# Optimization experiments

Measured on AMD Instinct MI355X. Metric: run time of the kernel, lower is better.

Reference implementation:

```python
import jax, jax.numpy as jnp
import numpy as np
from jax import lax

N, T, V, E, H, D, B = 16384, 16, 10000, 256, 256, 512, 128


def setup_inputs() -> dict:
    key = jax.random.key(0)
    ks = jax.random.split(key, 12)
    tok = jax.random.randint(ks[0], (N, T), 1, V)
    lens = jax.random.randint(ks[1], (N,), 4, T + 1)
    tok = jnp.where(jnp.arange(T)[None, :] < lens[:, None], tok, 0)  # pad_id = 0
    ast_path_len = jnp.full((B,), N // B, dtype=jnp.int32)  # 128 paths per sample
    u = lambda k, s: jax.random.uniform(k, s, jnp.float32, -0.1, 0.1)
    emb = u(ks[2], (V, E)).at[0].set(0.0)  # padding_idx=0 row zeroed
    return {
        "ast_path": tok,
        "ast_path_len": ast_path_len,
        "emb": emb,
        "W_ih_f": u(ks[3], (4 * H, E)), "W_hh_f": u(ks[4], (4 * H, H)), "b_f": u(ks[5], (4 * H,)),
        "W_ih_b": u(ks[6], (4 * H, E)), "W_hh_b": u(ks[7], (4 * H, H)), "b_b": u(ks[8], (4 * H,)),
        "W_lin": u(ks[9], (D, 2 * H)), "b_lin": jnp.zeros((D,), jnp.float32),
    }


def _lstm_final_h(x_tm, lens, W_ih, W_hh, b, reverse):
    # x_tm: [T, N, E]; returns final hidden state [N, H] honoring per-seq length
    n = x_tm.shape[1]
    h0 = jnp.zeros((n, H), x_tm.dtype)

    def step(carry, xt):
        h, c = carry
        x, t = xt
        gates = x @ W_ih.T + h @ W_hh.T + b  # [N, 4H]
        i, f, g, o = jnp.split(gates, 4, axis=-1)
        c_new = jax.nn.sigmoid(f) * c + jax.nn.sigmoid(i) * jnp.tanh(g)
        h_new = jax.nn.sigmoid(o) * jnp.tanh(c_new)
        m = (t < lens)[:, None]  # packed-sequence semantics: frozen past length
        return (jnp.where(m, h_new, h), jnp.where(m, c_new, c)), None

    (h, _), _ = lax.scan(step, (h0, h0), (x_tm, jnp.arange(x_tm.shape[0])), reverse=reverse)
    return h


def reference(ast_path, ast_path_len, emb, W_ih_f, W_hh_f, b_f, W_ih_b, W_hh_b, b_b, W_lin, b_lin):
    lens = (ast_path != 0).sum(axis=-1)  # pad_id = 0
    x = emb[ast_path]                     # [N, T, E]; dropout is identity at eval
    x_tm = jnp.swapaxes(x, 0, 1)          # [T, N, E]
    h_fwd = _lstm_final_h(x_tm, lens, W_ih_f, W_hh_f, b_f, reverse=False)
    h_bwd = _lstm_final_h(x_tm, lens, W_ih_b, W_hh_b, b_b, reverse=True)
    h_n = jnp.concatenate([h_fwd, h_bwd], axis=1)        # [N, 2H]
    repr_ = h_n @ W_lin.T + b_lin                         # [N, D]
    # segment-mean pooling over path groups (replaces the Python loop)
    n_paths = repr_.shape[0]
    seg_ids = jnp.repeat(jnp.arange(ast_path_len.shape[0]), ast_path_len,
                         total_repeat_length=n_paths)
    sums = jax.ops.segment_sum(repr_, seg_ids, num_segments=ast_path_len.shape[0])
    pooled = sums / ast_path_len[:, None].astype(repr_.dtype)  # [B, D]
    norm = jnp.sqrt(jnp.sum(pooled * pooled, axis=-1, keepdims=True))
    return pooled / jnp.maximum(norm, 1e-5)
```

## Files before the change

### kernel.cpp

```cpp
#include <hip/hip_runtime.h>
#include <stdint.h>

#define N_SEQ 16384
#define T_LEN 16
#define E_DIM 256
#define H_DIM 256
#define B_SAMP 128
#define V_SIZE 10000

typedef __bf16 bf16x8 __attribute__((ext_vector_type(8)));
typedef float  f32x4  __attribute__((ext_vector_type(4)));
typedef unsigned short u16x8 __attribute__((ext_vector_type(8)));
typedef unsigned short ush;

__device__ __forceinline__ ush f2bf(float x) {
  unsigned int u = __float_as_uint(x);
  u = (u + 0x7fffu + ((u >> 16) & 1u)) >> 16;
  return (ush)u;
}
__device__ __forceinline__ float bf2f(ush v) {
  return __uint_as_float(((unsigned int)v) << 16);
}
__device__ __forceinline__ float sigmoidf_(float x) {
  return 1.0f / (1.0f + __expf(-x));
}
__device__ __forceinline__ float tanhf_(float x) {
  float e = __expf(2.0f * x);
  return 1.0f - 2.0f / (e + 1.0f);
}
__device__ __forceinline__ void glds16(const void* g, const void* l) {
  __builtin_amdgcn_global_load_lds(
      (const __attribute__((address_space(1))) unsigned int*)g,
      (__attribute__((address_space(3))) unsigned int*)l, 16, 0, 0);
}


__global__ __launch_bounds__(256) void k_lens(const int* __restrict__ tok, int* __restrict__ lens) {
  int n = blockIdx.x * 256 + threadIdx.x;
  const int* r = tok + n * T_LEN;
  int c = 0;
#pragma unroll
  for (int t = 0; t < T_LEN; ++t) c += (r[t] != 0);
  lens[n] = c;
}

__global__ __launch_bounds__(256) void k_hist(const int* __restrict__ lens, int* __restrict__ hist) {
  __shared__ int lh[17];
  if (threadIdx.x < 17) lh[threadIdx.x] = 0;
  __syncthreads();
  atomicAdd(&lh[lens[blockIdx.x * 256 + threadIdx.x]], 1);
  __syncthreads();
  if (threadIdx.x < 17) atomicAdd(&hist[threadIdx.x], lh[threadIdx.x]);
}

__global__ void k_offsets(const int* __restrict__ hist, int* __restrict__ cursor,
                          int* __restrict__ cnts_f, int* __restrict__ cnts_b) {
  if (threadIdx.x == 0) {
    int off = 0;
    for (int l = 16; l >= 0; --l) { cursor[l] = off; off += hist[l]; }
    for (int t = 0; t < 16; ++t) {
      int cf = 0, cb = 0;
      for (int l = t; l <= 16; ++l) cf += hist[l];
      for (int l = t + 1; l <= 16; ++l) cb += hist[l];
      cnts_f[t] = cf;
      cnts_b[t] = cb;
    }
  }
}

__global__ __launch_bounds__(256) void k_scatter(const int* __restrict__ tok, const int* __restrict__ lens,
                                                 int* __restrict__ cursor,
                                                 int* __restrict__ pinv, int* __restrict__ plens,
                                                 int* __restrict__ tokperm) {
  int n = blockIdx.x * 256 + threadIdx.x;
  int l = lens[n];
  int pos = atomicAdd(&cursor[l], 1);
  pinv[n] = pos;
  plens[pos] = l;
#pragma unroll
  for (int t = 0; t < T_LEN; ++t) tokperm[t * N_SEQ + pos] = tok[n * T_LEN + t];
}

__global__ __launch_bounds__(256) void k_embcvt(const float* __restrict__ emb, ush* __restrict__ out) {
  int i = blockIdx.x * 256 + threadIdx.x;
  out[i] = f2bf(emb[i]);
}

__global__ __launch_bounds__(256) void k_wprep(const float* __restrict__ Wih_f, const float* __restrict__ Whh_f,
                                               const float* __restrict__ Wih_b, const float* __restrict__ Whh_b,
                                               ush* __restrict__ wihp_f, ush* __restrict__ wihp_b,
                                               ush* __restrict__ whhp_f, ush* __restrict__ whhp_b) {
  int id = blockIdx.x * 256 + threadIdx.x;
  int mat = id >> 19;
  int dir = (id >> 18) & 1;
  int rem = id & ((1 << 18) - 1);
  int p = rem >> 8;
  int k = rem & 255;
  int r = ((p >> 4) & 3) * 256 + (p >> 6) * 16 + (p & 15);
  const float* src = mat ? (dir ? Whh_b : Whh_f) : (dir ? Wih_b : Wih_f);
  ush* dst = mat ? (dir ? whhp_b : whhp_f) : (dir ? wihp_b : wihp_f);
  dst[p * 256 + k] = f2bf(src[r * 256 + k]);
}


__global__ __launch_bounds__(512, 4)
void k_vproj(const ush* __restrict__ embbf,
             const ush* __restrict__ wihp_f, const ush* __restrict__ wihp_b,
             float* __restrict__ proj_f, float* __restrict__ proj_b) {
  const int dir = blockIdx.y;
  const int wtile = blockIdx.x >> 2;
  const int nblk = blockIdx.x & 3;
  const int m0 = wtile * 128;
  const ush* wih = dir ? wihp_b : wihp_f;
  float* proj = dir ? proj_b : proj_f;

  __shared__ __align__(128) unsigned char ldsA[128 * 128];
  __shared__ __align__(128) unsigned char ldsB[256 * 128];

  const int tid = threadIdx.x;
  const int lane = tid & 63;
  const int w = tid >> 6;
  const int wr = w >> 2, wc = w & 3;
  const int l8 = lane >> 3, l7 = lane & 7;
  const int frow = lane & 15, fkq = lane >> 4;

  const int arow0 = 16 * w + l8, arow1 = arow0 + 8;
  const unsigned aoff0 = (unsigned)(m0 + arow0) * 256 + (l7 ^ (arow0 & 7)) * 8;
  const unsigned aoff1 = (unsigned)(m0 + arow1) * 256 + (l7 ^ (arow1 & 7)) * 8;
  unsigned boff[4];
#pragma unroll
  for (int j = 0; j < 4; ++j) {
    const int brow = 32 * w + 8 * j + l8;
    boff[j] = (unsigned)(nblk * 256 + brow) * 256 + (l7 ^ (brow & 7)) * 8;
  }

  f32x4 acc[4][4] = {};
  for (int kt = 0; kt < 4; ++kt) {
    const int k0 = kt * 64;
    glds16(embbf + aoff0 + k0, &ldsA[(16 * w) * 128]);
    glds16(embbf + aoff1 + k0, &ldsA[(16 * w + 8) * 128]);
#pragma unroll
    for (int j = 0; j < 4; ++j)
      glds16(wih + boff[j] + k0, &ldsB[(32 * w + 8 * j) * 128]);
    __syncthreads();
#pragma unroll
    for (int ksub = 0; ksub < 2; ++ksub) {
      bf16x8 av[4], bv[4];
#pragma unroll
      for (int fr = 0; fr < 4; ++fr) {
        const int row = wr * 64 + fr * 16 + frow;
        av[fr] = *(const bf16x8*)&ldsA[row * 128 + (((ksub * 4 + fkq) ^ (row & 7)) * 16)];
      }
#pragma unroll
      for (int fc = 0; fc < 4; ++fc) {
        const int row = wc * 64 + fc * 16 + frow;
        bv[fc] = *(const bf16x8*)&ldsB[row * 128 + (((ksub * 4 + fkq) ^ (row & 7)) * 16)];
      }
#pragma unroll
      for (int fr = 0; fr < 4; ++fr)
#pragma unroll
        for (int fc = 0; fc < 4; ++fc)
          acc[fr][fc] = __builtin_amdgcn_mfma_f32_16x16x32_bf16(av[fr], bv[fc], acc[fr][fc], 0, 0, 0);
    }
    __syncthreads();
  }

  const int pcb = nblk * 256 + wc * 64 + frow;
#pragma unroll
  for (int fr = 0; fr < 4; ++fr) {
    const int v0 = m0 + wr * 64 + fr * 16 + fkq * 4;
#pragma unroll
    for (int q = 0; q < 4; ++q)
#pragma unroll
      for (int r = 0; r < 4; ++r)
        if (v0 + r < V_SIZE) proj[(size_t)(v0 + r) * 1024 + pcb + q * 16] = acc[fr][q][r];
  }
}


__global__ __launch_bounds__(512, 4)
void k_step(const float* __restrict__ proj_f, const float* __restrict__ proj_b,
            const int* __restrict__ tokperm, const int* __restrict__ plens,
            const int* __restrict__ cnts_f, const int* __restrict__ cnts_b,
            const ush* __restrict__ whhp_f, const ush* __restrict__ whhp_b,
            const float* __restrict__ bias_f, const float* __restrict__ bias_b,
            const ush* __restrict__ hr_f, ush* __restrict__ hw_f,
            const ush* __restrict__ hr_b, ush* __restrict__ hw_b,
            float* __restrict__ cT_f, float* __restrict__ cT_b,
            int s) {
  const int dir = blockIdx.y;
  const int t = dir ? (15 - s) : s;
  const int cnt = dir ? cnts_b[t] : cnts_f[t];
  const int wtile = blockIdx.x >> 2;
  const int m0 = wtile * 128;
  if (m0 >= cnt) return;

  const int nblk = blockIdx.x & 3;
  const float* proj = dir ? proj_b : proj_f;
  const ush* whh = dir ? whhp_b : whhp_f;
  const float* bias = dir ? bias_b : bias_f;
  const ush* hr = dir ? hr_b : hr_f;
  ush* hw = dir ? hw_b : hw_f;
  float* cT = dir ? cT_b : cT_f;

  __shared__ __align__(128) unsigned char ldsA[128 * 128];
  __shared__ __align__(128) unsigned char ldsB[256 * 128];

  const int tid = threadIdx.x;
  const int lane = tid & 63;
  const int w = tid >> 6;
  const int wr = w >> 2, wc = w & 3;
  const int l8 = lane >> 3, l7 = lane & 7;
  const int frow = lane & 15, fkq = lane >> 4;

  const int arow0 = 16 * w + l8, arow1 = arow0 + 8;
  const unsigned aoff0 = (unsigned)(m0 + arow0) * 256 + (l7 ^ (arow0 & 7)) * 8;
  const unsigned aoff1 = (unsigned)(m0 + arow1) * 256 + (l7 ^ (arow1 & 7)) * 8;
  unsigned boff[4];
#pragma unroll
  for (int j = 0; j < 4; ++j) {
    const int brow = 32 * w + 8 * j + l8;
    boff[j] = (unsigned)(nblk * 256 + brow) * 256 + (l7 ^ (brow & 7)) * 8;
  }

  f32x4 acc[4][4] = {};
  for (int kt = 0; kt < 4; ++kt) {
    const int k0 = kt * 64;
    glds16(hr + aoff0 + k0, &ldsA[(16 * w) * 128]);
    glds16(hr + aoff1 + k0, &ldsA[(16 * w + 8) * 128]);
#pragma unroll
    for (int j = 0; j < 4; ++j)
      glds16(whh + boff[j] + k0, &ldsB[(32 * w + 8 * j) * 128]);
    __syncthreads();
#pragma unroll
    for (int ksub = 0; ksub < 2; ++ksub) {
      bf16x8 av[4], bv[4];
#pragma unroll
      for (int fr = 0; fr < 4; ++fr) {
        const int row = wr * 64 + fr * 16 + frow;
        av[fr] = *(const bf16x8*)&ldsA[row * 128 + (((ksub * 4 + fkq) ^ (row & 7)) * 16)];
      }
#pragma unroll
      for (int fc = 0; fc < 4; ++fc) {
        const int row = wc * 64 + fc * 16 + frow;
        bv[fc] = *(const bf16x8*)&ldsB[row * 128 + (((ksub * 4 + fkq) ^ (row & 7)) * 16)];
      }
#pragma unroll
      for (int fr = 0; fr < 4; ++fr)
#pragma unroll
        for (int fc = 0; fc < 4; ++fc)
          acc[fr][fc] = __builtin_amdgcn_mfma_f32_16x16x32_bf16(av[fr], bv[fc], acc[fr][fc], 0, 0, 0);
    }
    __syncthreads();
  }

  const int j = nblk * 64 + wc * 16 + frow;
  const int pcb = nblk * 256 + wc * 64 + frow;
  const float b0 = bias[j], b1 = bias[256 + j], b2 = bias[512 + j], b3 = bias[768 + j];
#pragma unroll
  for (int fr = 0; fr < 4; ++fr) {
    const int n0 = m0 + wr * 64 + fr * 16 + fkq * 4;
    const int4 l4 = *(const int4*)&plens[n0];
    const int4 tv = *(const int4*)&tokperm[t * N_SEQ + n0];
    f32x4 cv = *(f32x4*)&cT[(size_t)j * N_SEQ + n0];
    f32x4 gi = acc[fr][0], gf = acc[fr][1], gg = acc[fr][2], go = acc[fr][3];
#pragma unroll
    for (int r = 0; r < 4; ++r) {
      const int tvr = (r == 0) ? tv.x : (r == 1) ? tv.y : (r == 2) ? tv.z : tv.w;
      const float* pr = proj + (size_t)tvr * 1024 + pcb;
      gi[r] += b0 + pr[0];
      gf[r] += b1 + pr[16];
      gg[r] += b2 + pr[32];
      go[r] += b3 + pr[48];
    }
#pragma unroll
    for (int r = 0; r < 4; ++r) {
      const int lnv = (r == 0) ? l4.x : (r == 1) ? l4.y : (r == 2) ? l4.z : l4.w;
      const size_t hidx = (size_t)(n0 + r) * H_DIM + j;
      if (t < lnv) {
        const float iv = sigmoidf_(gi[r]);
        const float fv = sigmoidf_(gf[r]);
        const float gv = tanhf_(gg[r]);
        const float ov = sigmoidf_(go[r]);
        const float cn = fv * cv[r] + iv * gv;
        cv[r] = cn;
        hw[hidx] = f2bf(ov * tanhf_(cn));
      } else {
        hw[hidx] = hr[hidx];
      }
    }
    *(f32x4*)&cT[(size_t)j * N_SEQ + n0] = cv;
  }
}


__global__ __launch_bounds__(256) void k_pool(const ush* __restrict__ hf,
                                              const ush* __restrict__ hb,
                                              const int* __restrict__ pinv,
                                              const int* __restrict__ plen,
                                              float* __restrict__ pooled) {
  const int b = blockIdx.x, tid = threadIdx.x;
  int start = 0;
  for (int i = 0; i < b; ++i) start += plen[i];
  const int cnt = plen[b];
  float s0 = 0.f, s1 = 0.f;
  for (int r = 0; r < cnt; ++r) {
    const size_t pr = (size_t)pinv[start + r];
    s0 += bf2f(hf[pr * H_DIM + tid]);
    s1 += bf2f(hb[pr * H_DIM + tid]);
  }
  float inv = 1.0f / (float)cnt;
  pooled[b * 512 + tid] = s0 * inv;
  pooled[b * 512 + H_DIM + tid] = s1 * inv;
}


__global__ __launch_bounds__(256) void k_final(const float* __restrict__ pooled,
                                               const float* __restrict__ W,
                                               const float* __restrict__ bl,
                                               float* __restrict__ out) {
  const int b = blockIdx.x, tid = threadIdx.x;
  __shared__ float pv[512];
  __shared__ float pre[512];
  __shared__ float red[4];
  pv[tid] = pooled[b * 512 + tid];
  pv[tid + 256] = pooled[b * 512 + 256 + tid];
  __syncthreads();
#pragma unroll
  for (int half = 0; half < 2; ++half) {
    const int dd = tid + half * 256;
    const f32x4* wr = (const f32x4*)(W + (size_t)dd * 512);
    const f32x4* pvv = (const f32x4*)pv;
    float s = bl[dd];
#pragma unroll 4
    for (int k4 = 0; k4 < 128; ++k4) {
      f32x4 wv = wr[k4], xv = pvv[k4];
      s += wv[0] * xv[0] + wv[1] * xv[1] + wv[2] * xv[2] + wv[3] * xv[3];
    }
    pre[dd] = s;
  }
  __syncthreads();
  float ss = pre[tid] * pre[tid] + pre[tid + 256] * pre[tid + 256];
#pragma unroll
  for (int off = 32; off > 0; off >>= 1) ss += __shfl_down(ss, off, 64);
  if ((tid & 63) == 0) red[tid >> 6] = ss;
  __syncthreads();
  float tot = red[0] + red[1] + red[2] + red[3];
  float scale = 1.0f / fmaxf(sqrtf(tot), 1e-5f);
  out[b * 512 + tid] = pre[tid] * scale;
  out[b * 512 + 256 + tid] = pre[tid + 256] * scale;
}


extern "C" void kernel_launch(void* const* d_in, const int* in_sizes, int n_in,
                              void* d_out, int out_size, void* d_ws, size_t ws_size,
                              hipStream_t stream) {
  const int* tok    = (const int*)d_in[0];
  const int* plen   = (const int*)d_in[1];
  const float* emb  = (const float*)d_in[2];
  const float* Wih_f = (const float*)d_in[3];
  const float* Whh_f = (const float*)d_in[4];
  const float* b_f   = (const float*)d_in[5];
  const float* Wih_b = (const float*)d_in[6];
  const float* Whh_b = (const float*)d_in[7];
  const float* b_b   = (const float*)d_in[8];
  const float* Wlin  = (const float*)d_in[9];
  const float* blin  = (const float*)d_in[10];
  float* out = (float*)d_out;

  char* ws = (char*)d_ws;
  size_t off = 0;
  auto alloc = [&](size_t bytes) {
    void* p = ws + off;
    off = (off + bytes + 255) & ~(size_t)255;
    return p;
  };
  ush* embbf   = (ush*)alloc((size_t)V_SIZE * E_DIM * 2);
  ush* wihpf   = (ush*)alloc((size_t)1024 * 256 * 2);
  ush* wihpb   = (ush*)alloc((size_t)1024 * 256 * 2);
  ush* whhpf   = (ush*)alloc((size_t)1024 * 256 * 2);
  ush* whhpb   = (ush*)alloc((size_t)1024 * 256 * 2);
  int* lens    = (int*)alloc((size_t)N_SEQ * 4);
  int* pinv    = (int*)alloc((size_t)N_SEQ * 4);
  int* plens   = (int*)alloc((size_t)N_SEQ * 4);
  int* tokperm = (int*)alloc((size_t)T_LEN * N_SEQ * 4);
  int* hist    = (int*)alloc(17 * 4);
  int* cursor  = (int*)alloc(17 * 4);
  int* cntsf   = (int*)alloc(16 * 4);
  int* cntsb   = (int*)alloc(16 * 4);
  float* projf = (float*)alloc((size_t)V_SIZE * 1024 * 4);
  float* projb = (float*)alloc((size_t)V_SIZE * 1024 * 4);
  ush* h0f     = (ush*)alloc((size_t)N_SEQ * H_DIM * 2);
  ush* h1f     = (ush*)alloc((size_t)N_SEQ * H_DIM * 2);
  ush* h0b     = (ush*)alloc((size_t)N_SEQ * H_DIM * 2);
  ush* h1b     = (ush*)alloc((size_t)N_SEQ * H_DIM * 2);
  float* cTf   = (float*)alloc((size_t)H_DIM * N_SEQ * 4);
  float* cTb   = (float*)alloc((size_t)H_DIM * N_SEQ * 4);
  float* pooled = (float*)alloc((size_t)B_SAMP * 512 * 4);

  hipMemsetAsync(hist, 0, 17 * 4, stream);
  hipMemsetAsync(h0f, 0, (size_t)N_SEQ * H_DIM * 2, stream);
  hipMemsetAsync(h1f, 0, (size_t)N_SEQ * H_DIM * 2, stream);
  hipMemsetAsync(h0b, 0, (size_t)N_SEQ * H_DIM * 2, stream);
  hipMemsetAsync(h1b, 0, (size_t)N_SEQ * H_DIM * 2, stream);
  hipMemsetAsync(cTf, 0, (size_t)H_DIM * N_SEQ * 4, stream);
  hipMemsetAsync(cTb, 0, (size_t)H_DIM * N_SEQ * 4, stream);

  k_lens<<<N_SEQ / 256, 256, 0, stream>>>(tok, lens);
  k_hist<<<N_SEQ / 256, 256, 0, stream>>>(lens, hist);
  k_offsets<<<1, 64, 0, stream>>>(hist, cursor, cntsf, cntsb);
  k_scatter<<<N_SEQ / 256, 256, 0, stream>>>(tok, lens, cursor, pinv, plens, tokperm);
  k_embcvt<<<(V_SIZE * E_DIM) / 256, 256, 0, stream>>>(emb, embbf);
  k_wprep<<<(2 * 2 * 1024 * 256) / 256, 256, 0, stream>>>(Wih_f, Whh_f, Wih_b, Whh_b,
                                                           wihpf, wihpb, whhpf, whhpb);
  k_vproj<<<dim3(79 * 4, 2), 512, 0, stream>>>(embbf, wihpf, wihpb, projf, projb);

  dim3 grid(512, 2);
  for (int s = 0; s < T_LEN; ++s) {
    const ush* hrf = (s & 1) ? h1f : h0f;
    ush* hwf       = (s & 1) ? h0f : h1f;
    const ush* hrb = (s & 1) ? h1b : h0b;
    ush* hwb       = (s & 1) ? h0b : h1b;
    k_step<<<grid, 512, 0, stream>>>(projf, projb, tokperm, plens, cntsf, cntsb,
                                     whhpf, whhpb, b_f, b_b,
                                     hrf, hwf, hrb, hwb, cTf, cTb, s);
  }
  k_pool<<<B_SAMP, 256, 0, stream>>>(h0f, h0b, pinv, plen, pooled);
  k_final<<<B_SAMP, 256, 0, stream>>>(pooled, Wlin, blin, out);
}
```

Baseline: 923.8 us.

## Retile LSTM GEMMs with double-buffered LDS, fold bias into projection, fuse setup kernels

```diff
diff --git a/kernel.cpp b/kernel.cpp
--- a/kernel.cpp
+++ b/kernel.cpp
@@ -10,7 +10,6 @@
 
 typedef __bf16 bf16x8 __attribute__((ext_vector_type(8)));
 typedef float  f32x4  __attribute__((ext_vector_type(4)));
-typedef unsigned short u16x8 __attribute__((ext_vector_type(8)));
 typedef unsigned short ush;
 
 __device__ __forceinline__ ush f2bf(float x) {
@@ -35,22 +34,20 @@
 }
 
 
-__global__ __launch_bounds__(256) void k_lens(const int* __restrict__ tok, int* __restrict__ lens) {
+__global__ __launch_bounds__(256) void k_lens(const int* __restrict__ tok, int* __restrict__ lens,
+                                              int* __restrict__ hist) {
+  __shared__ int lh[17];
+  if (threadIdx.x < 17) lh[threadIdx.x] = 0;
+  __syncthreads();
   int n = blockIdx.x * 256 + threadIdx.x;
   const int* r = tok + n * T_LEN;
   int c = 0;
 #pragma unroll
   for (int t = 0; t < T_LEN; ++t) c += (r[t] != 0);
   lens[n] = c;
-}
-
-__global__ __launch_bounds__(256) void k_hist(const int* __restrict__ lens, int* __restrict__ hist) {
-  __shared__ int lh[17];
-  if (threadIdx.x < 17) lh[threadIdx.x] = 0;
-  __syncthreads();
-  atomicAdd(&lh[lens[blockIdx.x * 256 + threadIdx.x]], 1);
-  __syncthreads();
-  if (threadIdx.x < 17) atomicAdd(&hist[threadIdx.x], lh[threadIdx.x]);
+  atomicAdd(&lh[c], 1);
+  __syncthreads();
+  if (threadIdx.x < 17 && lh[threadIdx.x]) atomicAdd(&hist[threadIdx.x], lh[threadIdx.x]);
 }
 
 __global__ void k_offsets(const int* __restrict__ hist, int* __restrict__ cursor,
@@ -68,17 +65,23 @@
   }
 }
 
-__global__ __launch_bounds__(256) void k_scatter(const int* __restrict__ tok, const int* __restrict__ lens,
-                                                 int* __restrict__ cursor,
-                                                 int* __restrict__ pinv, int* __restrict__ plens,
-                                                 int* __restrict__ tokperm) {
+__global__ __launch_bounds__(256) void k_scatter(const int* __restrict__ lens, int* __restrict__ cursor,
+                                                 int* __restrict__ perm, int* __restrict__ pinv,
+                                                 int* __restrict__ plens) {
   int n = blockIdx.x * 256 + threadIdx.x;
   int l = lens[n];
   int pos = atomicAdd(&cursor[l], 1);
+  perm[pos] = n;
   pinv[n] = pos;
   plens[pos] = l;
-#pragma unroll
-  for (int t = 0; t < T_LEN; ++t) tokperm[t * N_SEQ + pos] = tok[n * T_LEN + t];
+}
+
+__global__ __launch_bounds__(256) void k_tokperm(const int* __restrict__ tok, const int* __restrict__ perm,
+                                                 int* __restrict__ tokperm) {
+  int id = blockIdx.x * 256 + threadIdx.x;
+  int t = id >> 14;
+  int pos = id & (N_SEQ - 1);
+  tokperm[id] = tok[perm[pos] * T_LEN + t];
 }
 
 __global__ __launch_bounds__(256) void k_embcvt(const float* __restrict__ emb, ush* __restrict__ out) {
@@ -96,65 +99,69 @@
   int rem = id & ((1 << 18) - 1);
   int p = rem >> 8;
   int k = rem & 255;
-  int r = ((p >> 4) & 3) * 256 + (p >> 6) * 16 + (p & 15);
+  int nb = p >> 7, wc = (p >> 6) & 1, q = (p >> 4) & 3, jj = p & 15;
+  int j = nb * 32 + wc * 16 + jj;
+  int r = q * 256 + j;
   const float* src = mat ? (dir ? Whh_b : Whh_f) : (dir ? Wih_b : Wih_f);
   ush* dst = mat ? (dir ? whhp_b : whhp_f) : (dir ? wihp_b : wihp_f);
   dst[p * 256 + k] = f2bf(src[r * 256 + k]);
 }
 
 
-__global__ __launch_bounds__(512, 4)
+__global__ __launch_bounds__(256, 2)
 void k_vproj(const ush* __restrict__ embbf,
              const ush* __restrict__ wihp_f, const ush* __restrict__ wihp_b,
+             const float* __restrict__ bias_f, const float* __restrict__ bias_b,
              float* __restrict__ proj_f, float* __restrict__ proj_b) {
   const int dir = blockIdx.y;
-  const int wtile = blockIdx.x >> 2;
-  const int nblk = blockIdx.x & 3;
-  const int m0 = wtile * 128;
+  const int vt = blockIdx.x >> 3;
+  const int nb = blockIdx.x & 7;
+  const int m0 = vt * 128;
   const ush* wih = dir ? wihp_b : wihp_f;
+  const float* bias = dir ? bias_b : bias_f;
   float* proj = dir ? proj_b : proj_f;
 
-  __shared__ __align__(128) unsigned char ldsA[128 * 128];
-  __shared__ __align__(128) unsigned char ldsB[256 * 128];
+  __shared__ __align__(128) unsigned char ldsA[2][16384];
+  __shared__ __align__(128) unsigned char ldsB[2][16384];
 
   const int tid = threadIdx.x;
   const int lane = tid & 63;
   const int w = tid >> 6;
-  const int wr = w >> 2, wc = w & 3;
+  const int wr = w >> 1, wc = w & 1;
   const int l8 = lane >> 3, l7 = lane & 7;
   const int frow = lane & 15, fkq = lane >> 4;
 
-  const int arow0 = 16 * w + l8, arow1 = arow0 + 8;
-  const unsigned aoff0 = (unsigned)(m0 + arow0) * 256 + (l7 ^ (arow0 & 7)) * 8;
-  const unsigned aoff1 = (unsigned)(m0 + arow1) * 256 + (l7 ^ (arow1 & 7)) * 8;
-  unsigned boff[4];
-#pragma unroll
-  for (int j = 0; j < 4; ++j) {
-    const int brow = 32 * w + 8 * j + l8;
-    boff[j] = (unsigned)(nblk * 256 + brow) * 256 + (l7 ^ (brow & 7)) * 8;
-  }
-
   f32x4 acc[4][4] = {};
-  for (int kt = 0; kt < 4; ++kt) {
+
+  auto stage = [&](int b, int kt) {
     const int k0 = kt * 64;
-    glds16(embbf + aoff0 + k0, &ldsA[(16 * w) * 128]);
-    glds16(embbf + aoff1 + k0, &ldsA[(16 * w + 8) * 128]);
-#pragma unroll
-    for (int j = 0; j < 4; ++j)
-      glds16(wih + boff[j] + k0, &ldsB[(32 * w + 8 * j) * 128]);
-    __syncthreads();
+#pragma unroll
+    for (int i = 0; i < 4; ++i) {
+      const int arow = 32 * w + 8 * i + l8;
+      glds16(embbf + (size_t)(m0 + arow) * 256 + k0 + ((l7 ^ (arow & 7)) * 8),
+             &ldsA[b][(32 * w + 8 * i) * 128]);
+    }
+#pragma unroll
+    for (int i = 0; i < 4; ++i) {
+      const int brow = 32 * w + 8 * i + l8;
+      glds16(wih + (size_t)(nb * 128 + brow) * 256 + k0 + ((l7 ^ (brow & 7)) * 8),
+             &ldsB[b][(32 * w + 8 * i) * 128]);
+    }
+  };
+  auto compute = [&](int b) {
 #pragma unroll
     for (int ksub = 0; ksub < 2; ++ksub) {
+      const int slot = ksub * 4 + fkq;
       bf16x8 av[4], bv[4];
 #pragma unroll
       for (int fr = 0; fr < 4; ++fr) {
         const int row = wr * 64 + fr * 16 + frow;
-        av[fr] = *(const bf16x8*)&ldsA[row * 128 + (((ksub * 4 + fkq) ^ (row & 7)) * 16)];
+        av[fr] = *(const bf16x8*)&ldsA[b][row * 128 + ((slot ^ (row & 7)) * 16)];
       }
 #pragma unroll
       for (int fc = 0; fc < 4; ++fc) {
-        const int row = wc * 64 + fc * 16 + frow;
-        bv[fc] = *(const bf16x8*)&ldsB[row * 128 + (((ksub * 4 + fkq) ^ (row & 7)) * 16)];
+        const int prow = wc * 64 + fc * 16 + frow;
+        bv[fc] = *(const bf16x8*)&ldsB[b][prow * 128 + ((slot ^ (prow & 7)) * 16)];
       }
 #pragma unroll
       for (int fr = 0; fr < 4; ++fr)
@@ -162,28 +169,38 @@
         for (int fc = 0; fc < 4; ++fc)
           acc[fr][fc] = __builtin_amdgcn_mfma_f32_16x16x32_bf16(av[fr], bv[fc], acc[fr][fc], 0, 0, 0);
     }
+  };
+
+  stage(0, 0);
+  __syncthreads();
+#pragma unroll
+  for (int kt = 0; kt < 4; ++kt) {
+    if (kt < 3) stage((kt + 1) & 1, kt + 1);
+    compute(kt & 1);
     __syncthreads();
   }
 
-  const int pcb = nblk * 256 + wc * 64 + frow;
+  const int j = nb * 32 + wc * 16 + frow;
+  const f32x4 pb = {bias[j], bias[256 + j], bias[512 + j], bias[768 + j]};
 #pragma unroll
   for (int fr = 0; fr < 4; ++fr) {
     const int v0 = m0 + wr * 64 + fr * 16 + fkq * 4;
 #pragma unroll
-    for (int q = 0; q < 4; ++q)
-#pragma unroll
-      for (int r = 0; r < 4; ++r)
-        if (v0 + r < V_SIZE) proj[(size_t)(v0 + r) * 1024 + pcb + q * 16] = acc[fr][q][r];
-  }
-}
-
-
-__global__ __launch_bounds__(512, 4)
+    for (int r = 0; r < 4; ++r) {
+      if (v0 + r < V_SIZE) {
+        f32x4 v4 = {acc[fr][0][r], acc[fr][1][r], acc[fr][2][r], acc[fr][3][r]};
+        *(f32x4*)&proj[(size_t)(v0 + r) * 1024 + j * 4] = v4 + pb;
+      }
+    }
+  }
+}
+
+
+__global__ __launch_bounds__(256, 2)
 void k_step(const float* __restrict__ proj_f, const float* __restrict__ proj_b,
             const int* __restrict__ tokperm, const int* __restrict__ plens,
             const int* __restrict__ cnts_f, const int* __restrict__ cnts_b,
             const ush* __restrict__ whhp_f, const ush* __restrict__ whhp_b,
-            const float* __restrict__ bias_f, const float* __restrict__ bias_b,
             const ush* __restrict__ hr_f, ush* __restrict__ hw_f,
             const ush* __restrict__ hr_b, ush* __restrict__ hw_b,
             float* __restrict__ cT_f, float* __restrict__ cT_b,
@@ -191,59 +208,58 @@
   const int dir = blockIdx.y;
   const int t = dir ? (15 - s) : s;
   const int cnt = dir ? cnts_b[t] : cnts_f[t];
-  const int wtile = blockIdx.x >> 2;
-  const int m0 = wtile * 128;
+  const int rt = blockIdx.x >> 3;
+  const int m0 = rt * 128;
   if (m0 >= cnt) return;
 
-  const int nblk = blockIdx.x & 3;
+  const int nb = blockIdx.x & 7;
   const float* proj = dir ? proj_b : proj_f;
   const ush* whh = dir ? whhp_b : whhp_f;
-  const float* bias = dir ? bias_b : bias_f;
   const ush* hr = dir ? hr_b : hr_f;
   ush* hw = dir ? hw_b : hw_f;
   float* cT = dir ? cT_b : cT_f;
 
-  __shared__ __align__(128) unsigned char ldsA[128 * 128];
-  __shared__ __align__(128) unsigned char ldsB[256 * 128];
+  __shared__ __align__(128) unsigned char ldsA[2][16384];
+  __shared__ __align__(128) unsigned char ldsB[2][16384];
 
   const int tid = threadIdx.x;
   const int lane = tid & 63;
   const int w = tid >> 6;
-  const int wr = w >> 2, wc = w & 3;
+  const int wr = w >> 1, wc = w & 1;
   const int l8 = lane >> 3, l7 = lane & 7;
   const int frow = lane & 15, fkq = lane >> 4;
 
-  const int arow0 = 16 * w + l8, arow1 = arow0 + 8;
-  const unsigned aoff0 = (unsigned)(m0 + arow0) * 256 + (l7 ^ (arow0 & 7)) * 8;
-  const unsigned aoff1 = (unsigned)(m0 + arow1) * 256 + (l7 ^ (arow1 & 7)) * 8;
-  unsigned boff[4];
-#pragma unroll
-  for (int j = 0; j < 4; ++j) {
-    const int brow = 32 * w + 8 * j + l8;
-    boff[j] = (unsigned)(nblk * 256 + brow) * 256 + (l7 ^ (brow & 7)) * 8;
-  }
-
   f32x4 acc[4][4] = {};
-  for (int kt = 0; kt < 4; ++kt) {
+
+  auto stage = [&](int b, int kt) {
     const int k0 = kt * 64;
-    glds16(hr + aoff0 + k0, &ldsA[(16 * w) * 128]);
-    glds16(hr + aoff1 + k0, &ldsA[(16 * w + 8) * 128]);
-#pragma unroll
-    for (int j = 0; j < 4; ++j)
-      glds16(whh + boff[j] + k0, &ldsB[(32 * w + 8 * j) * 128]);
-    __syncthreads();
+#pragma unroll
+    for (int i = 0; i < 4; ++i) {
+      const int arow = 32 * w + 8 * i + l8;
+      glds16(hr + (size_t)(m0 + arow) * 256 + k0 + ((l7 ^ (arow & 7)) * 8),
+             &ldsA[b][(32 * w + 8 * i) * 128]);
+    }
+#pragma unroll
+    for (int i = 0; i < 4; ++i) {
+      const int brow = 32 * w + 8 * i + l8;
+      glds16(whh + (size_t)(nb * 128 + brow) * 256 + k0 + ((l7 ^ (brow & 7)) * 8),
+             &ldsB[b][(32 * w + 8 * i) * 128]);
+    }
+  };
+  auto compute = [&](int b) {
 #pragma unroll
     for (int ksub = 0; ksub < 2; ++ksub) {
+      const int slot = ksub * 4 + fkq;
       bf16x8 av[4], bv[4];
 #pragma unroll
       for (int fr = 0; fr < 4; ++fr) {
         const int row = wr * 64 + fr * 16 + frow;
-        av[fr] = *(const bf16x8*)&ldsA[row * 128 + (((ksub * 4 + fkq) ^ (row & 7)) * 16)];
+        av[fr] = *(const bf16x8*)&ldsA[b][row * 128 + ((slot ^ (row & 7)) * 16)];
       }
 #pragma unroll
       for (int fc = 0; fc < 4; ++fc) {
-        const int row = wc * 64 + fc * 16 + frow;
-        bv[fc] = *(const bf16x8*)&ldsB[row * 128 + (((ksub * 4 + fkq) ^ (row & 7)) * 16)];
+        const int prow = wc * 64 + fc * 16 + frow;
+        bv[fc] = *(const bf16x8*)&ldsB[b][prow * 128 + ((slot ^ (prow & 7)) * 16)];
       }
 #pragma unroll
       for (int fr = 0; fr < 4; ++fr)
@@ -251,41 +267,40 @@
         for (int fc = 0; fc < 4; ++fc)
           acc[fr][fc] = __builtin_amdgcn_mfma_f32_16x16x32_bf16(av[fr], bv[fc], acc[fr][fc], 0, 0, 0);
     }
+  };
+
+  stage(0, 0);
+  __syncthreads();
+#pragma unroll
+  for (int kt = 0; kt < 4; ++kt) {
+    if (kt < 3) stage((kt + 1) & 1, kt + 1);
+    compute(kt & 1);
     __syncthreads();
   }
 
-  const int j = nblk * 64 + wc * 16 + frow;
-  const int pcb = nblk * 256 + wc * 64 + frow;
-  const float b0 = bias[j], b1 = bias[256 + j], b2 = bias[512 + j], b3 = bias[768 + j];
+  const int j = nb * 32 + wc * 16 + frow;
 #pragma unroll
   for (int fr = 0; fr < 4; ++fr) {
     const int n0 = m0 + wr * 64 + fr * 16 + fkq * 4;
     const int4 l4 = *(const int4*)&plens[n0];
     const int4 tv = *(const int4*)&tokperm[t * N_SEQ + n0];
-    f32x4 cv = *(f32x4*)&cT[(size_t)j * N_SEQ + n0];
-    f32x4 gi = acc[fr][0], gf = acc[fr][1], gg = acc[fr][2], go = acc[fr][3];
-#pragma unroll
-    for (int r = 0; r < 4; ++r) {
-      const int tvr = (r == 0) ? tv.x : (r == 1) ? tv.y : (r == 2) ? tv.z : tv.w;
-      const float* pr = proj + (size_t)tvr * 1024 + pcb;
-      gi[r] += b0 + pr[0];
-      gf[r] += b1 + pr[16];
-      gg[r] += b2 + pr[32];
-      go[r] += b3 + pr[48];
-    }
+    f32x4 cv = *(const f32x4*)&cT[(size_t)j * N_SEQ + n0];
 #pragma unroll
     for (int r = 0; r < 4; ++r) {
       const int lnv = (r == 0) ? l4.x : (r == 1) ? l4.y : (r == 2) ? l4.z : l4.w;
+      const int tvr = (r == 0) ? tv.x : (r == 1) ? tv.y : (r == 2) ? tv.z : tv.w;
       const size_t hidx = (size_t)(n0 + r) * H_DIM + j;
       if (t < lnv) {
-        const float iv = sigmoidf_(gi[r]);
-        const float fv = sigmoidf_(gf[r]);
-        const float gv = tanhf_(gg[r]);
-        const float ov = sigmoidf_(go[r]);
-        const float cn = fv * cv[r] + iv * gv;
+        const f32x4 pr4 = *(const f32x4*)&proj[(size_t)tvr * 1024 + j * 4];
+        const float iv = sigmoidf_(acc[fr][0][r] + pr4[0]);
+        const float fv = sigmoidf_(acc[fr][1][r] + pr4[1]);
+        const float gv = tanhf_(acc[fr][2][r] + pr4[2]);
+        const float ov = sigmoidf_(acc[fr][3][r] + pr4[3]);
+        const bool first = dir ? (t == lnv - 1) : (t == 0);
+        const float cn = fv * (first ? 0.0f : cv[r]) + iv * gv;
         cv[r] = cn;
         hw[hidx] = f2bf(ov * tanhf_(cn));
-      } else {
+      } else if (!dir) {
         hw[hidx] = hr[hidx];
       }
     }
@@ -381,6 +396,7 @@
   ush* whhpf   = (ush*)alloc((size_t)1024 * 256 * 2);
   ush* whhpb   = (ush*)alloc((size_t)1024 * 256 * 2);
   int* lens    = (int*)alloc((size_t)N_SEQ * 4);
+  int* perm    = (int*)alloc((size_t)N_SEQ * 4);
   int* pinv    = (int*)alloc((size_t)N_SEQ * 4);
   int* plens   = (int*)alloc((size_t)N_SEQ * 4);
   int* tokperm = (int*)alloc((size_t)T_LEN * N_SEQ * 4);
@@ -403,27 +419,24 @@
   hipMemsetAsync(h1f, 0, (size_t)N_SEQ * H_DIM * 2, stream);
   hipMemsetAsync(h0b, 0, (size_t)N_SEQ * H_DIM * 2, stream);
   hipMemsetAsync(h1b, 0, (size_t)N_SEQ * H_DIM * 2, stream);
-  hipMemsetAsync(cTf, 0, (size_t)H_DIM * N_SEQ * 4, stream);
-  hipMemsetAsync(cTb, 0, (size_t)H_DIM * N_SEQ * 4, stream);
-
-  k_lens<<<N_SEQ / 256, 256, 0, stream>>>(tok, lens);
-  k_hist<<<N_SEQ / 256, 256, 0, stream>>>(lens, hist);
+
+  k_lens<<<N_SEQ / 256, 256, 0, stream>>>(tok, lens, hist);
   k_offsets<<<1, 64, 0, stream>>>(hist, cursor, cntsf, cntsb);
-  k_scatter<<<N_SEQ / 256, 256, 0, stream>>>(tok, lens, cursor, pinv, plens, tokperm);
+  k_scatter<<<N_SEQ / 256, 256, 0, stream>>>(lens, cursor, perm, pinv, plens);
+  k_tokperm<<<(T_LEN * N_SEQ) / 256, 256, 0, stream>>>(tok, perm, tokperm);
   k_embcvt<<<(V_SIZE * E_DIM) / 256, 256, 0, stream>>>(emb, embbf);
   k_wprep<<<(2 * 2 * 1024 * 256) / 256, 256, 0, stream>>>(Wih_f, Whh_f, Wih_b, Whh_b,
                                                            wihpf, wihpb, whhpf, whhpb);
-  k_vproj<<<dim3(79 * 4, 2), 512, 0, stream>>>(embbf, wihpf, wihpb, projf, projb);
-
-  dim3 grid(512, 2);
+  k_vproj<<<dim3(79 * 8, 2), 256, 0, stream>>>(embbf, wihpf, wihpb, b_f, b_b, projf, projb);
+
+  dim3 grid(128 * 8, 2);
   for (int s = 0; s < T_LEN; ++s) {
     const ush* hrf = (s & 1) ? h1f : h0f;
     ush* hwf       = (s & 1) ? h0f : h1f;
     const ush* hrb = (s & 1) ? h1b : h0b;
     ush* hwb       = (s & 1) ? h0b : h1b;
-    k_step<<<grid, 512, 0, stream>>>(projf, projb, tokperm, plens, cntsf, cntsb,
-                                     whhpf, whhpb, b_f, b_b,
-                                     hrf, hwf, hrb, hwb, cTf, cTb, s);
+    k_step<<<grid, 256, 0, stream>>>(projf, projb, tokperm, plens, cntsf, cntsb,
+                                     whhpf, whhpb, hrf, hwf, hrb, hwb, cTf, cTb, s);
   }
   k_pool<<<B_SAMP, 256, 0, stream>>>(h0f, h0b, pinv, plen, pooled);
   k_final<<<B_SAMP, 256, 0, stream>>>(pooled, Wlin, blin, out);
```

New measurement: 1.057 ms. 14.4% more time.

## Fold bias into vocab projection, skip finished rows, and interleave LSTM step grid

Applied to the files above, without the earlier changes.

```diff
diff --git a/kernel.cpp b/kernel.cpp
--- a/kernel.cpp
+++ b/kernel.cpp
@@ -10,7 +10,6 @@
 
 typedef __bf16 bf16x8 __attribute__((ext_vector_type(8)));
 typedef float  f32x4  __attribute__((ext_vector_type(4)));
-typedef unsigned short u16x8 __attribute__((ext_vector_type(8)));
 typedef unsigned short ush;
 
 __device__ __forceinline__ ush f2bf(float x) {
@@ -35,50 +34,52 @@
 }
 
 
-__global__ __launch_bounds__(256) void k_lens(const int* __restrict__ tok, int* __restrict__ lens) {
+__global__ __launch_bounds__(256) void k_lens(const int* __restrict__ tok, int* __restrict__ lens,
+                                              int* __restrict__ hist) {
+  __shared__ int lh[17];
+  if (threadIdx.x < 17) lh[threadIdx.x] = 0;
+  __syncthreads();
   int n = blockIdx.x * 256 + threadIdx.x;
   const int* r = tok + n * T_LEN;
   int c = 0;
 #pragma unroll
   for (int t = 0; t < T_LEN; ++t) c += (r[t] != 0);
   lens[n] = c;
-}
-
-__global__ __launch_bounds__(256) void k_hist(const int* __restrict__ lens, int* __restrict__ hist) {
-  __shared__ int lh[17];
-  if (threadIdx.x < 17) lh[threadIdx.x] = 0;
+  atomicAdd(&lh[c], 1);
   __syncthreads();
-  atomicAdd(&lh[lens[blockIdx.x * 256 + threadIdx.x]], 1);
-  __syncthreads();
-  if (threadIdx.x < 17) atomicAdd(&hist[threadIdx.x], lh[threadIdx.x]);
+  if (threadIdx.x < 17 && lh[threadIdx.x]) atomicAdd(&hist[threadIdx.x], lh[threadIdx.x]);
 }
 
 __global__ void k_offsets(const int* __restrict__ hist, int* __restrict__ cursor,
-                          int* __restrict__ cnts_f, int* __restrict__ cnts_b) {
+                          int* __restrict__ cnts) {
   if (threadIdx.x == 0) {
     int off = 0;
     for (int l = 16; l >= 0; --l) { cursor[l] = off; off += hist[l]; }
     for (int t = 0; t < 16; ++t) {
-      int cf = 0, cb = 0;
-      for (int l = t; l <= 16; ++l) cf += hist[l];
-      for (int l = t + 1; l <= 16; ++l) cb += hist[l];
-      cnts_f[t] = cf;
-      cnts_b[t] = cb;
-    }
-  }
-}
-
-__global__ __launch_bounds__(256) void k_scatter(const int* __restrict__ tok, const int* __restrict__ lens,
-                                                 int* __restrict__ cursor,
-                                                 int* __restrict__ pinv, int* __restrict__ plens,
-                                                 int* __restrict__ tokperm) {
+      int c = 0;
+      for (int l = t + 1; l <= 16; ++l) c += hist[l];
+      cnts[t] = c;
+    }
+  }
+}
+
+__global__ __launch_bounds__(256) void k_scatter(const int* __restrict__ lens, int* __restrict__ cursor,
+                                                 int* __restrict__ perm, int* __restrict__ pinv,
+                                                 int* __restrict__ plens) {
   int n = blockIdx.x * 256 + threadIdx.x;
   int l = lens[n];
   int pos = atomicAdd(&cursor[l], 1);
+  perm[pos] = n;
   pinv[n] = pos;
   plens[pos] = l;
-#pragma unroll
-  for (int t = 0; t < T_LEN; ++t) tokperm[t * N_SEQ + pos] = tok[n * T_LEN + t];
+}
+
+__global__ __launch_bounds__(256) void k_tokperm(const int* __restrict__ tok, const int* __restrict__ perm,
+                                                 int* __restrict__ tokperm) {
+  int id = blockIdx.x * 256 + threadIdx.x;
+  int t = id >> 14;
+  int pos = id & (N_SEQ - 1);
+  tokperm[id] = tok[perm[pos] * T_LEN + t];
 }
 
 __global__ __launch_bounds__(256) void k_embcvt(const float* __restrict__ emb, ush* __restrict__ out) {
@@ -96,7 +97,8 @@
   int rem = id & ((1 << 18) - 1);
   int p = rem >> 8;
   int k = rem & 255;
-  int r = ((p >> 4) & 3) * 256 + (p >> 6) * 16 + (p & 15);
+  int nb = p >> 8, wc = (p >> 6) & 3, q = (p >> 4) & 3, jj = p & 15;
+  int r = q * 256 + nb * 64 + wc * 16 + jj;
   const float* src = mat ? (dir ? Whh_b : Whh_f) : (dir ? Wih_b : Wih_f);
   ush* dst = mat ? (dir ? whhp_b : whhp_f) : (dir ? wihp_b : wihp_f);
   dst[p * 256 + k] = f2bf(src[r * 256 + k]);
@@ -106,12 +108,14 @@
 __global__ __launch_bounds__(512, 4)
 void k_vproj(const ush* __restrict__ embbf,
              const ush* __restrict__ wihp_f, const ush* __restrict__ wihp_b,
+             const float* __restrict__ bias_f, const float* __restrict__ bias_b,
              float* __restrict__ proj_f, float* __restrict__ proj_b) {
   const int dir = blockIdx.y;
-  const int wtile = blockIdx.x >> 2;
+  const int vt = blockIdx.x >> 2;
   const int nblk = blockIdx.x & 3;
-  const int m0 = wtile * 128;
+  const int m0 = vt * 128;
   const ush* wih = dir ? wihp_b : wihp_f;
+  const float* bias = dir ? bias_b : bias_f;
   float* proj = dir ? proj_b : proj_f;
 
   __shared__ __align__(128) unsigned char ldsA[128 * 128];
@@ -129,9 +133,9 @@
   const unsigned aoff1 = (unsigned)(m0 + arow1) * 256 + (l7 ^ (arow1 & 7)) * 8;
   unsigned boff[4];
 #pragma unroll
-  for (int j = 0; j < 4; ++j) {
-    const int brow = 32 * w + 8 * j + l8;
-    boff[j] = (unsigned)(nblk * 256 + brow) * 256 + (l7 ^ (brow & 7)) * 8;
+  for (int jj = 0; jj < 4; ++jj) {
+    const int brow = 32 * w + 8 * jj + l8;
+    boff[jj] = (unsigned)(nblk * 256 + brow) * 256 + (l7 ^ (brow & 7)) * 8;
   }
 
   f32x4 acc[4][4] = {};
@@ -140,8 +144,8 @@
     glds16(embbf + aoff0 + k0, &ldsA[(16 * w) * 128]);
     glds16(embbf + aoff1 + k0, &ldsA[(16 * w + 8) * 128]);
 #pragma unroll
-    for (int j = 0; j < 4; ++j)
-      glds16(wih + boff[j] + k0, &ldsB[(32 * w + 8 * j) * 128]);
+    for (int jj = 0; jj < 4; ++jj)
+      glds16(wih + boff[jj] + k0, &ldsB[(32 * w + 8 * jj) * 128]);
     __syncthreads();
 #pragma unroll
     for (int ksub = 0; ksub < 2; ++ksub) {
@@ -165,15 +169,18 @@
     __syncthreads();
   }
 
-  const int pcb = nblk * 256 + wc * 64 + frow;
+  const int j = nblk * 64 + wc * 16 + frow;
+  const f32x4 pb = {bias[j], bias[256 + j], bias[512 + j], bias[768 + j]};
 #pragma unroll
   for (int fr = 0; fr < 4; ++fr) {
     const int v0 = m0 + wr * 64 + fr * 16 + fkq * 4;
 #pragma unroll
-    for (int q = 0; q < 4; ++q)
-#pragma unroll
-      for (int r = 0; r < 4; ++r)
-        if (v0 + r < V_SIZE) proj[(size_t)(v0 + r) * 1024 + pcb + q * 16] = acc[fr][q][r];
+    for (int r = 0; r < 4; ++r) {
+      if (v0 + r < V_SIZE) {
+        f32x4 v4 = {acc[fr][0][r], acc[fr][1][r], acc[fr][2][r], acc[fr][3][r]};
+        *(f32x4*)&proj[(size_t)(v0 + r) * 1024 + j * 4] = v4 + pb;
+      }
+    }
   }
 }
 
@@ -181,24 +188,23 @@
 __global__ __launch_bounds__(512, 4)
 void k_step(const float* __restrict__ proj_f, const float* __restrict__ proj_b,
             const int* __restrict__ tokperm, const int* __restrict__ plens,
-            const int* __restrict__ cnts_f, const int* __restrict__ cnts_b,
+            const int* __restrict__ cnts,
             const ush* __restrict__ whhp_f, const ush* __restrict__ whhp_b,
-            const float* __restrict__ bias_f, const float* __restrict__ bias_b,
             const ush* __restrict__ hr_f, ush* __restrict__ hw_f,
             const ush* __restrict__ hr_b, ush* __restrict__ hw_b,
             float* __restrict__ cT_f, float* __restrict__ cT_b,
             int s) {
-  const int dir = blockIdx.y;
+  const int b = blockIdx.x;
+  const int dir = b & 1;
+  const int nblk = (b & 7) >> 1;
+  const int rt = b >> 3;
   const int t = dir ? (15 - s) : s;
-  const int cnt = dir ? cnts_b[t] : cnts_f[t];
-  const int wtile = blockIdx.x >> 2;
-  const int m0 = wtile * 128;
+  const int cnt = cnts[t];
+  const int m0 = rt * 128;
   if (m0 >= cnt) return;
 
-  const int nblk = blockIdx.x & 3;
   const float* proj = dir ? proj_b : proj_f;
   const ush* whh = dir ? whhp_b : whhp_f;
-  const float* bias = dir ? bias_b : bias_f;
   const ush* hr = dir ? hr_b : hr_f;
   ush* hw = dir ? hw_b : hw_f;
   float* cT = dir ? cT_b : cT_f;
@@ -213,14 +219,25 @@
   const int l8 = lane >> 3, l7 = lane & 7;
   const int frow = lane & 15, fkq = lane >> 4;
 
+  const int j = nblk * 64 + wc * 16 + frow;
+  int4 l4[4], tv4[4];
+  f32x4 cv4[4];
+#pragma unroll
+  for (int fr = 0; fr < 4; ++fr) {
+    const int n0 = m0 + wr * 64 + fr * 16 + fkq * 4;
+    l4[fr] = *(const int4*)&plens[n0];
+    tv4[fr] = *(const int4*)&tokperm[t * N_SEQ + n0];
+    cv4[fr] = *(const f32x4*)&cT[(size_t)j * N_SEQ + n0];
+  }
+
   const int arow0 = 16 * w + l8, arow1 = arow0 + 8;
   const unsigned aoff0 = (unsigned)(m0 + arow0) * 256 + (l7 ^ (arow0 & 7)) * 8;
   const unsigned aoff1 = (unsigned)(m0 + arow1) * 256 + (l7 ^ (arow1 & 7)) * 8;
   unsigned boff[4];
 #pragma unroll
-  for (int j = 0; j < 4; ++j) {
-    const int brow = 32 * w + 8 * j + l8;
-    boff[j] = (unsigned)(nblk * 256 + brow) * 256 + (l7 ^ (brow & 7)) * 8;
+  for (int jj = 0; jj < 4; ++jj) {
+    const int brow = 32 * w + 8 * jj + l8;
+    boff[jj] = (unsigned)(nblk * 256 + brow) * 256 + (l7 ^ (brow & 7)) * 8;
   }
 
   f32x4 acc[4][4] = {};
@@ -229,8 +246,8 @@
     glds16(hr + aoff0 + k0, &ldsA[(16 * w) * 128]);
     glds16(hr + aoff1 + k0, &ldsA[(16 * w + 8) * 128]);
 #pragma unroll
-    for (int j = 0; j < 4; ++j)
-      glds16(whh + boff[j] + k0, &ldsB[(32 * w + 8 * j) * 128]);
+    for (int jj = 0; jj < 4; ++jj)
+      glds16(whh + boff[jj] + k0, &ldsB[(32 * w + 8 * jj) * 128]);
     __syncthreads();
 #pragma unroll
     for (int ksub = 0; ksub < 2; ++ksub) {
@@ -245,48 +262,40 @@
         const int row = wc * 64 + fc * 16 + frow;
         bv[fc] = *(const bf16x8*)&ldsB[row * 128 + (((ksub * 4 + fkq) ^ (row & 7)) * 16)];
       }
+      __builtin_amdgcn_s_setprio(1);
 #pragma unroll
       for (int fr = 0; fr < 4; ++fr)
 #pragma unroll
         for (int fc = 0; fc < 4; ++fc)
           acc[fr][fc] = __builtin_amdgcn_mfma_f32_16x16x32_bf16(av[fr], bv[fc], acc[fr][fc], 0, 0, 0);
+      __builtin_amdgcn_s_setprio(0);
     }
     __syncthreads();
   }
 
-  const int j = nblk * 64 + wc * 16 + frow;
-  const int pcb = nblk * 256 + wc * 64 + frow;
-  const float b0 = bias[j], b1 = bias[256 + j], b2 = bias[512 + j], b3 = bias[768 + j];
 #pragma unroll
   for (int fr = 0; fr < 4; ++fr) {
     const int n0 = m0 + wr * 64 + fr * 16 + fkq * 4;
-    const int4 l4 = *(const int4*)&plens[n0];
-    const int4 tv = *(const int4*)&tokperm[t * N_SEQ + n0];
-    f32x4 cv = *(f32x4*)&cT[(size_t)j * N_SEQ + n0];
-    f32x4 gi = acc[fr][0], gf = acc[fr][1], gg = acc[fr][2], go = acc[fr][3];
+    const int4 ln = tv4[fr];
+    const int4 lv = l4[fr];
+    const int lmax = max(max(lv.x, lv.y), max(lv.z, lv.w));
+    if (t >= lmax) continue;
+    f32x4 cv = cv4[fr];
+    const f32x4 gi = acc[fr][0], gf = acc[fr][1], gg = acc[fr][2], go = acc[fr][3];
 #pragma unroll
     for (int r = 0; r < 4; ++r) {
-      const int tvr = (r == 0) ? tv.x : (r == 1) ? tv.y : (r == 2) ? tv.z : tv.w;
-      const float* pr = proj + (size_t)tvr * 1024 + pcb;
-      gi[r] += b0 + pr[0];
-      gf[r] += b1 + pr[16];
-      gg[r] += b2 + pr[32];
-      go[r] += b3 + pr[48];
-    }
-#pragma unroll
-    for (int r = 0; r < 4; ++r) {
-      const int lnv = (r == 0) ? l4.x : (r == 1) ? l4.y : (r == 2) ? l4.z : l4.w;
-      const size_t hidx = (size_t)(n0 + r) * H_DIM + j;
+      const int lnv = (r == 0) ? lv.x : (r == 1) ? lv.y : (r == 2) ? lv.z : lv.w;
       if (t < lnv) {
-        const float iv = sigmoidf_(gi[r]);
-        const float fv = sigmoidf_(gf[r]);
-        const float gv = tanhf_(gg[r]);
-        const float ov = sigmoidf_(go[r]);
-        const float cn = fv * cv[r] + iv * gv;
+        const int tvr = (r == 0) ? ln.x : (r == 1) ? ln.y : (r == 2) ? ln.z : ln.w;
+        const f32x4 pr4 = *(const f32x4*)&proj[(size_t)tvr * 1024 + j * 4];
+        const float iv = sigmoidf_(gi[r] + pr4[0]);
+        const float fv = sigmoidf_(gf[r] + pr4[1]);
+        const float gv = tanhf_(gg[r] + pr4[2]);
+        const float ov = sigmoidf_(go[r] + pr4[3]);
+        const bool first = dir ? (t == lnv - 1) : (t == 0);
+        const float cn = fv * (first ? 0.0f : cv[r]) + iv * gv;
         cv[r] = cn;
-        hw[hidx] = f2bf(ov * tanhf_(cn));
-      } else {
-        hw[hidx] = hr[hidx];
+        hw[(size_t)(n0 + r) * H_DIM + j] = f2bf(ov * tanhf_(cn));
       }
     }
     *(f32x4*)&cT[(size_t)j * N_SEQ + n0] = cv;
@@ -294,9 +303,9 @@
 }
 
 
-__global__ __launch_bounds__(256) void k_pool(const ush* __restrict__ hf,
-                                              const ush* __restrict__ hb,
-                                              const int* __restrict__ pinv,
+__global__ __launch_bounds__(256) void k_pool(const ush* __restrict__ h0f, const ush* __restrict__ h1f,
+                                              const ush* __restrict__ h0b,
+                                              const int* __restrict__ pinv, const int* __restrict__ lens,
                                               const int* __restrict__ plen,
                                               float* __restrict__ pooled) {
   const int b = blockIdx.x, tid = threadIdx.x;
@@ -305,9 +314,12 @@
   const int cnt = plen[b];
   float s0 = 0.f, s1 = 0.f;
   for (int r = 0; r < cnt; ++r) {
-    const size_t pr = (size_t)pinv[start + r];
+    const int n = start + r;
+    const size_t pr = (size_t)pinv[n];
+    const int l = lens[n];
+    const ush* hf = (l & 1) ? h1f : h0f;
     s0 += bf2f(hf[pr * H_DIM + tid]);
-    s1 += bf2f(hb[pr * H_DIM + tid]);
+    s1 += bf2f(h0b[pr * H_DIM + tid]);
   }
   float inv = 1.0f / (float)cnt;
   pooled[b * 512 + tid] = s0 * inv;
@@ -381,13 +393,13 @@
   ush* whhpf   = (ush*)alloc((size_t)1024 * 256 * 2);
   ush* whhpb   = (ush*)alloc((size_t)1024 * 256 * 2);
   int* lens    = (int*)alloc((size_t)N_SEQ * 4);
+  int* perm    = (int*)alloc((size_t)N_SEQ * 4);
   int* pinv    = (int*)alloc((size_t)N_SEQ * 4);
   int* plens   = (int*)alloc((size_t)N_SEQ * 4);
   int* tokperm = (int*)alloc((size_t)T_LEN * N_SEQ * 4);
   int* hist    = (int*)alloc(17 * 4);
   int* cursor  = (int*)alloc(17 * 4);
-  int* cntsf   = (int*)alloc(16 * 4);
-  int* cntsb   = (int*)alloc(16 * 4);
+  int* cnts    = (int*)alloc(16 * 4);
   float* projf = (float*)alloc((size_t)V_SIZE * 1024 * 4);
   float* projb = (float*)alloc((size_t)V_SIZE * 1024 * 4);
   ush* h0f     = (ush*)alloc((size_t)N_SEQ * H_DIM * 2);
@@ -403,28 +415,24 @@
   hipMemsetAsync(h1f, 0, (size_t)N_SEQ * H_DIM * 2, stream);
   hipMemsetAsync(h0b, 0, (size_t)N_SEQ * H_DIM * 2, stream);
   hipMemsetAsync(h1b, 0, (size_t)N_SEQ * H_DIM * 2, stream);
-  hipMemsetAsync(cTf, 0, (size_t)H_DIM * N_SEQ * 4, stream);
-  hipMemsetAsync(cTb, 0, (size_t)H_DIM * N_SEQ * 4, stream);
-
-  k_lens<<<N_SEQ / 256, 256, 0, stream>>>(tok, lens);
-  k_hist<<<N_SEQ / 256, 256, 0, stream>>>(lens, hist);
-  k_offsets<<<1, 64, 0, stream>>>(hist, cursor, cntsf, cntsb);
-  k_scatter<<<N_SEQ / 256, 256, 0, stream>>>(tok, lens, cursor, pinv, plens, tokperm);
+
+  k_lens<<<N_SEQ / 256, 256, 0, stream>>>(tok, lens, hist);
+  k_offsets<<<1, 64, 0, stream>>>(hist, cursor, cnts);
+  k_scatter<<<N_SEQ / 256, 256, 0, stream>>>(lens, cursor, perm, pinv, plens);
+  k_tokperm<<<(T_LEN * N_SEQ) / 256, 256, 0, stream>>>(tok, perm, tokperm);
   k_embcvt<<<(V_SIZE * E_DIM) / 256, 256, 0, stream>>>(emb, embbf);
   k_wprep<<<(2 * 2 * 1024 * 256) / 256, 256, 0, stream>>>(Wih_f, Whh_f, Wih_b, Whh_b,
                                                            wihpf, wihpb, whhpf, whhpb);
-  k_vproj<<<dim3(79 * 4, 2), 512, 0, stream>>>(embbf, wihpf, wihpb, projf, projb);
-
-  dim3 grid(512, 2);
+  k_vproj<<<dim3(79 * 4, 2), 512, 0, stream>>>(embbf, wihpf, wihpb, b_f, b_b, projf, projb);
+
   for (int s = 0; s < T_LEN; ++s) {
     const ush* hrf = (s & 1) ? h1f : h0f;
     ush* hwf       = (s & 1) ? h0f : h1f;
     const ush* hrb = (s & 1) ? h1b : h0b;
     ush* hwb       = (s & 1) ? h0b : h1b;
-    k_step<<<grid, 512, 0, stream>>>(projf, projb, tokperm, plens, cntsf, cntsb,
-                                     whhpf, whhpb, b_f, b_b,
+    k_step<<<1024, 512, 0, stream>>>(projf, projb, tokperm, plens, cnts, whhpf, whhpb,
                                      hrf, hwf, hrb, hwb, cTf, cTb, s);
   }
-  k_pool<<<B_SAMP, 256, 0, stream>>>(h0f, h0b, pinv, plen, pooled);
+  k_pool<<<B_SAMP, 256, 0, stream>>>(h0f, h1f, h0b, pinv, lens, plen, pooled);
   k_final<<<B_SAMP, 256, 0, stream>>>(pooled, Wlin, blin, out);
 }
```

Result: slower. 1.269 ms (+37.4%).
